# Kernel tuning notes

Hardware: AMD Instinct MI355X
Metric: run time of the kernel (lower is better)

Reference implementation:

```python
import jax, jax.numpy as jnp
import numpy as np

S = 2   # scale_factor
K = 5   # k_up
M = 48  # m_channels
KE = 3  # k_encoder


def conv2d(x, w, b, pad):
    # NCHW conv, stride 1, symmetric padding (matches nn.Conv2d(padding=pad))
    y = jax.lax.conv_general_dilated(
        x, w, window_strides=(1, 1), padding=[(pad, pad), (pad, pad)],
        dimension_numbers=("NCHW", "OIHW", "NCHW"))
    return y + b[None, :, None, None]


def setup_inputs() -> dict:
    key = jax.random.key(0)
    k1, k2, k3, k4, k5 = jax.random.split(key, 5)
    C_in = 64
    x = jax.random.normal(k1, (8, C_in, 128, 128), dtype=jnp.float32)
    w_compress = jax.random.normal(k2, (M, C_in, 1, 1), dtype=jnp.float32) * 0.1
    b_compress = jax.random.normal(k3, (M,), dtype=jnp.float32) * 0.05
    w_encoder = jax.random.normal(k4, ((K * S) ** 2, M, KE, KE), dtype=jnp.float32) * 0.05
    b_encoder = jax.random.normal(k5, ((K * S) ** 2,), dtype=jnp.float32) * 0.05
    return {"x": x, "w_compress": w_compress, "b_compress": b_compress,
            "w_encoder": w_encoder, "b_encoder": b_encoder}


def reference(x, w_compress, b_compress, w_encoder, b_encoder):
    B, C, H, W = x.shape
    # mask branch: compress -> relu -> encoder -> softmax over k_up^2
    y = jax.nn.relu(conv2d(x, w_compress, b_compress, pad=0))
    y = conv2d(y, w_encoder, b_encoder, pad=KE // 2)          # [B, (K*S)^2, H, W]
    y = y.reshape(B, S * S, K * K, H, W)
    y = jax.nn.softmax(y, axis=2)
    # unfold x with kernel K, pad K//2, stride 1 -> [B, C, K*K, H, W]
    p = K // 2
    xpad = jnp.pad(x, ((0, 0), (0, 0), (p, p), (p, p)))
    unf = jnp.stack([xpad[:, :, i:i + H, j:j + W]
                     for i in range(K) for j in range(K)], axis=2)
    # per-subpixel softmax-weighted patch sum; channel layout (scale_idx, C)
    out = jnp.einsum("bskhw,bckhw->bschw", y, unf)            # [B, S^2, C, H, W]
    out = out.reshape(B, S * S * C, H, W)
    # PixelShuffle(S): view (B, C_out, r, r, H, W) -> (B, C_out, H, r, W, r)
    r = S
    c_out = (S * S * C) // (r * r)
    out = out.reshape(B, c_out, r, r, H, W).transpose(0, 1, 4, 2, 5, 3)
    return out.reshape(B, c_out, H * r, W * r)
```

## Files before the change

### kernel.cpp

```cpp
#include <hip/hip_runtime.h>

#define HW 16384

typedef __bf16 bf16x8 __attribute__((ext_vector_type(8)));
typedef __bf16 bf16x4 __attribute__((ext_vector_type(4)));
typedef float  f32x4  __attribute__((ext_vector_type(4)));
typedef float  f32x2  __attribute__((ext_vector_type(2)));

__global__ __launch_bounds__(256)
void prep_xt(const float* __restrict__ x, __bf16* __restrict__ xt) {
    __shared__ float lds[256 * 65];
    const int b = blockIdx.x & 7, chunk = blockIdx.x >> 3;
    const int t = threadIdx.x;
    const int pos0 = chunk * 256;
    const float* xb = x + (size_t)b * 64 * HW + pos0;
    for (int c = 0; c < 64; ++c)
        lds[t * 65 + c] = xb[(size_t)c * HW + t];
    __syncthreads();
    const int q = t & 3, pp = t >> 2;
    #pragma unroll
    for (int it = 0; it < 4; ++it) {
        int pos = it * 64 + pp;
        __bf16* o = xt + ((size_t)b * HW + pos0 + pos) * 64 + q * 16;
        bf16x8 v0, v1;
        #pragma unroll
        for (int e = 0; e < 8; ++e) {
            v0[e] = (__bf16)lds[pos * 65 + q * 16 + e];
            v1[e] = (__bf16)lds[pos * 65 + q * 16 + 8 + e];
        }
        *(bf16x8*)o       = v0;
        *(bf16x8*)(o + 8) = v1;
    }
}

__global__ __launch_bounds__(256)
void prep_w(const float* __restrict__ we, const float* __restrict__ wc,
            __bf16* __restrict__ wt, __bf16* __restrict__ wcb) {
    int idx = blockIdx.x * 256 + threadIdx.x;
    if (idx < 112 * 448) {
        int e = idx / 448, k = idx % 448;
        float v = 0.f;
        if (e < 100 && k < 432) {
            int t = k / 48, m = k % 48;
            v = we[(e * 48 + m) * 9 + t];
        }
        wt[idx] = (__bf16)v;
    } else {
        idx -= 112 * 448;
        if (idx < 48 * 64) wcb[idx] = (__bf16)wc[idx];
    }
}

__global__ __launch_bounds__(256, 2)
void carafe_weights(const __bf16* __restrict__ xt,
                    const __bf16* __restrict__ wcb, const float* __restrict__ bc,
                    const __bf16* __restrict__ wt, const float* __restrict__ be,
                    unsigned int* __restrict__ wnp) {
    __shared__ __align__(16) char smem[59392];
    __bf16*    y1  = (__bf16*)smem;
    _Float16*  lgt = (_Float16*)smem;

    const int tid = threadIdx.x;
    const int lane = tid & 63, wv = tid >> 6;
    const int lgp = lane >> 4, lr = lane & 15;
    const int b = blockIdx.x & 7, tile = blockIdx.x >> 3;
    const int h0 = (tile >> 3) << 4, w0 = (tile & 7) << 4;

    {
        bf16x8 bw[3][2];
        float bias1[3];
        #pragma unroll
        for (int nt = 0; nt < 3; ++nt) {
            bias1[nt] = bc[nt * 16 + lr];
            #pragma unroll
            for (int kc = 0; kc < 2; ++kc)
                bw[nt][kc] = *(const bf16x8*)(wcb + (nt * 16 + lr) * 64 + kc * 32 + lgp * 8);
        }
        for (int pt = wv; pt < 21; pt += 4) {
            int pos = pt * 16 + lr;
            int pr = (pos * 1821) >> 15;  int pc = pos - pr * 18;
            int hy = h0 - 1 + pr, wx = w0 - 1 + pc;
            bool ok = (hy >= 0) & (hy < 128) & (wx >= 0) & (wx < 128);
            const __bf16* ap = xt + ((size_t)b * HW + (ok ? (hy * 128 + wx) : 0)) * 64 + lgp * 8;
            bf16x8 a0 = *(const bf16x8*)ap;
            bf16x8 a1 = *(const bf16x8*)(ap + 32);
            if (!ok) {
                #pragma unroll
                for (int e = 0; e < 8; ++e) { a0[e] = (__bf16)0.f; a1[e] = (__bf16)0.f; }
            }
            #pragma unroll
            for (int nt = 0; nt < 3; ++nt) {
                f32x4 cc = {bias1[nt], bias1[nt], bias1[nt], bias1[nt]};
                cc = __builtin_amdgcn_mfma_f32_16x16x32_bf16(a0, bw[nt][0], cc, 0, 0, 0);
                cc = __builtin_amdgcn_mfma_f32_16x16x32_bf16(a1, bw[nt][1], cc, 0, 0, 0);
                #pragma unroll
                for (int r = 0; r < 4; ++r) {
                    int posw = pt * 16 + lgp * 4 + r;
                    int pr2 = (posw * 1821) >> 15;  int pc2 = posw - pr2 * 18;
                    int hy2 = h0 - 1 + pr2, wx2 = w0 - 1 + pc2;
                    bool ok2 = (hy2 >= 0) & (hy2 < 128) & (wx2 >= 0) & (wx2 < 128);
                    float v = ok2 ? fmaxf(cc[r], 0.f) : 0.f;
                    y1[posw * 56 + nt * 16 + lr] = (__bf16)v;
                }
            }
        }
    }
    for (int i = tid; i < 448; i += 256)
        y1[336 * 56 + i] = (__bf16)0.f;
    __syncthreads();

    f32x4 acc[4][7];
    #pragma unroll
    for (int ot = 0; ot < 7; ++ot) {
        int o_ = ot * 16 + lr;
        float bz = (o_ < 100) ? be[o_] : 0.f;
        #pragma unroll
        for (int i = 0; i < 4; ++i) acc[i][ot] = {bz, bz, bz, bz};
    }
    const int ptg0 = wv * 4;

    auto ldA = [&](bf16x8 A[4], int kc) {
        int Kb = kc * 32 + lgp * 8;
        int t  = (Kb * 683) >> 15;  int m0 = Kb - t * 48;
        int ty = (t * 11) >> 5;     int tx = t - ty * 3;
        int base = ty * 18 + lr + tx;
        #pragma unroll
        for (int i = 0; i < 4; ++i)
            A[i] = *(const bf16x8*)(y1 + ((ptg0 + i) * 18 + base) * 56 + m0);
    };
    auto ldB = [&](bf16x8 B[7], int kc) {
        #pragma unroll
        for (int j = 0; j < 7; ++j)
            B[j] = *(const bf16x8*)(wt + (j * 16 + lr) * 448 + kc * 32 + lgp * 8);
    };
    auto mm = [&](bf16x8 A[4], bf16x8 B[7]) {
        #pragma unroll
        for (int i = 0; i < 4; ++i)
            #pragma unroll
            for (int j = 0; j < 7; ++j)
                acc[i][j] = __builtin_amdgcn_mfma_f32_16x16x32_bf16(A[i], B[j], acc[i][j], 0, 0, 0);
    };

    bf16x8 A0[4], B0[7], A1[4], B1[7];
    ldA(A0, 0); ldB(B0, 0);
    #pragma unroll
    for (int kc = 0; kc < 14; kc += 2) {
        if (kc + 1 < 14) { ldA(A1, kc + 1); ldB(B1, kc + 1); }
        mm(A0, B0);
        if (kc + 2 < 14) { ldA(A0, kc + 2); ldB(B0, kc + 2); }
        if (kc + 1 < 14) mm(A1, B1);
    }
    __syncthreads();

    #pragma unroll
    for (int i = 0; i < 4; ++i)
        #pragma unroll
        for (int j = 0; j < 7; ++j) {
            int o_ = j * 16 + lr;
            #pragma unroll
            for (int r = 0; r < 4; ++r) {
                int p = (ptg0 + i) * 16 + lgp * 4 + r;
                lgt[p * 116 + o_] = (_Float16)acc[i][j][r];
            }
        }
    __syncthreads();

    const int p = tid;
    const _Float16* lrow = lgt + p * 116;
    #pragma unroll
    for (int s2 = 0; s2 < 2; ++s2) {
        unsigned int* wp = wnp + (size_t)(b * 2 + s2) * 25 * HW + tile * 256 + p;
        #pragma unroll
        for (int k = 0; k < 25; ++k) {
            unsigned short lo = __builtin_bit_cast(unsigned short, lrow[(2 * s2) * 25 + k]);
            unsigned short hi = __builtin_bit_cast(unsigned short, lrow[(2 * s2 + 1) * 25 + k]);
            wp[(size_t)k * HW] = (unsigned int)lo | ((unsigned int)hi << 16);
        }
    }
}

__global__ __launch_bounds__(512, 4)
void carafe_apply(const __bf16* __restrict__ xt, const unsigned int* __restrict__ wnp,
                  float* __restrict__ out) {
    __shared__ __bf16 lx[400 * 68];

    const int tid = threadIdx.x;
    const int b = blockIdx.x & 7, tile = blockIdx.x >> 3;
    const int h0 = (tile >> 3) << 4, w0 = (tile & 7) << 4;

    const int l8 = tid & 7, pg = tid >> 3;
    bf16x8 hv[7];
    #pragma unroll
    for (int it = 0; it < 7; ++it) {
        int pos = it * 64 + pg;
        bf16x8 v = {};
        if (pos < 400) {
            int r = pos / 20, q = pos % 20;
            int hy = h0 - 2 + r, wx = w0 - 2 + q;
            if (hy >= 0 && hy < 128 && wx >= 0 && wx < 128)
                v = *(const bf16x8*)(xt + ((size_t)b * HW + hy * 128 + wx) * 64 + l8 * 8);
        }
        hv[it] = v;
    }

    const int pix = tid & 255, sgrp = tid >> 8;
    const int py = pix >> 4, px = pix & 15;
    const int h = h0 + py, w = w0 + px;
    float wt_[50];
    {
        const unsigned int* wp = wnp + (size_t)(b * 2 + sgrp) * 25 * HW + tile * 256 + pix;
        #pragma unroll
        for (int k = 0; k < 25; ++k) {
            unsigned int u = wp[(size_t)k * HW];
            wt_[k]      = (float)__builtin_bit_cast(_Float16, (unsigned short)(u & 0xffffu));
            wt_[25 + k] = (float)__builtin_bit_cast(_Float16, (unsigned short)(u >> 16));
        }
        #pragma unroll
        for (int g = 0; g < 2; ++g) {
            float* v = wt_ + g * 25;
            float mx = v[0];
            #pragma unroll
            for (int k = 1; k < 25; ++k) mx = fmaxf(mx, v[k]);
            float s = 0.f;
            #pragma unroll
            for (int k = 0; k < 25; ++k) { v[k] = __expf(v[k] - mx); s += v[k]; }
            float inv = 1.f / s;
            #pragma unroll
            for (int k = 0; k < 25; ++k) v[k] *= inv;
        }
    }

    #pragma unroll
    for (int it = 0; it < 7; ++it) {
        int pos = it * 64 + pg;
        if (pos < 400) {
            bf16x4 vlo = {hv[it][0], hv[it][1], hv[it][2], hv[it][3]};
            bf16x4 vhi = {hv[it][4], hv[it][5], hv[it][6], hv[it][7]};
            *(bf16x4*)(lx + pos * 68 + l8 * 8)     = vlo;
            *(bf16x4*)(lx + pos * 68 + l8 * 8 + 4) = vhi;
        }
    }
    __syncthreads();

    float* ob = out + (size_t)b * 256 * HW;
    #pragma unroll 1
    for (int cq = 0; cq < 16; ++cq) {
        f32x2 a0 = {0.f, 0.f}, a1 = {0.f, 0.f}, a2 = {0.f, 0.f}, a3 = {0.f, 0.f};
        #pragma unroll
        for (int ki = 0; ki < 5; ++ki) {
            const int rowbase = (py + ki) * 20 + px;
            #pragma unroll
            for (int kj = 0; kj < 5; ++kj) {
                uint2 u = *(const uint2*)(lx + (rowbase + kj) * 68 + cq * 4);
                f32x2 xlo = { __uint_as_float(u.x << 16), __uint_as_float(u.x & 0xffff0000u) };
                f32x2 xhi = { __uint_as_float(u.y << 16), __uint_as_float(u.y & 0xffff0000u) };
                float wA = wt_[ki * 5 + kj];
                float wB = wt_[25 + ki * 5 + kj];
                a0 += xlo * wA;
                a1 += xhi * wA;
                a2 += xlo * wB;
                a3 += xhi * wB;
            }
        }
        size_t base0 = ((size_t)(sgrp * 32 + cq) * 256 + 2 * h) * 256 + 2 * w;
        *(f32x2*)(ob + base0)       = a0;
        *(f32x2*)(ob + base0 + 256) = a1;
        size_t base1 = base0 + (size_t)16 * 256 * 256;
        *(f32x2*)(ob + base1)       = a2;
        *(f32x2*)(ob + base1 + 256) = a3;
    }
}

extern "C" void kernel_launch(void* const* d_in, const int* in_sizes, int n_in,
                              void* d_out, int out_size, void* d_ws, size_t ws_size,
                              hipStream_t stream) {
    const float* x  = (const float*)d_in[0];
    const float* wc = (const float*)d_in[1];
    const float* bc = (const float*)d_in[2];
    const float* we = (const float*)d_in[3];
    const float* be = (const float*)d_in[4];
    float* out = (float*)d_out;

    __bf16*       xt  = (__bf16*)d_ws;
    __bf16*       wte = (__bf16*)((char*)d_ws + 16777216);
    __bf16*       wcb = (__bf16*)((char*)d_ws + 16777216 + 100352);
    unsigned int* wnp = (unsigned int*)((char*)d_ws + 16883712);

    prep_xt<<<512, 256, 0, stream>>>(x, xt);
    prep_w<<<208, 256, 0, stream>>>(we, wc, wte, wcb);
    carafe_weights<<<512, 256, 0, stream>>>(xt, wcb, bc, wte, be, wnp);
    carafe_apply<<<512, 512, 0, stream>>>(xt, wnp, out);
}
```

Baseline: 92.64 us.

## Split encoder output channels across two blocks per tile to raise occupancy

The weights kernel now launches twice as many blocks, each computing half of the 100 encoder outputs (two subpixel groups) for a tile, cutting accumulators from 4x7 to 4x4 MFMA tiles and shrinking LDS so four blocks fit per CU. The compress stage is transposed so each lane writes four contiguous channels with a vector store and reuses the load-time bounds check. The output stores in the apply kernel become nontemporal. The cost is that each half recomputes the compress conv and reloads the input halo, and the software double-buffering of the K loop is replaced by a plain unroll-by-two loop.

```diff
diff --git a/kernel.cpp b/kernel.cpp
--- a/kernel.cpp
+++ b/kernel.cpp
@@ -37,7 +37,7 @@
 void prep_w(const float* __restrict__ we, const float* __restrict__ wc,
             __bf16* __restrict__ wt, __bf16* __restrict__ wcb) {
     int idx = blockIdx.x * 256 + threadIdx.x;
-    if (idx < 112 * 448) {
+    if (idx < 128 * 448) {
         int e = idx / 448, k = idx % 448;
         float v = 0.f;
         if (e < 100 && k < 432) {
@@ -46,32 +46,34 @@
         }
         wt[idx] = (__bf16)v;
     } else {
-        idx -= 112 * 448;
+        idx -= 128 * 448;
         if (idx < 48 * 64) wcb[idx] = (__bf16)wc[idx];
     }
 }
 
-__global__ __launch_bounds__(256, 2)
+__global__ __launch_bounds__(256, 4)
 void carafe_weights(const __bf16* __restrict__ xt,
                     const __bf16* __restrict__ wcb, const float* __restrict__ bc,
                     const __bf16* __restrict__ wt, const float* __restrict__ be,
                     unsigned int* __restrict__ wnp) {
-    __shared__ __align__(16) char smem[59392];
+    __shared__ __align__(16) char smem[38528];
     __bf16*    y1  = (__bf16*)smem;
     _Float16*  lgt = (_Float16*)smem;
 
     const int tid = threadIdx.x;
     const int lane = tid & 63, wv = tid >> 6;
     const int lgp = lane >> 4, lr = lane & 15;
-    const int b = blockIdx.x & 7, tile = blockIdx.x >> 3;
+    const int b = blockIdx.x & 7;
+    const int rst = blockIdx.x >> 3;
+    const int tile = rst >> 1, half = rst & 1;
     const int h0 = (tile >> 3) << 4, w0 = (tile & 7) << 4;
 
     {
         bf16x8 bw[3][2];
-        float bias1[3];
+        f32x4 bias4[3];
         #pragma unroll
         for (int nt = 0; nt < 3; ++nt) {
-            bias1[nt] = bc[nt * 16 + lr];
+            bias4[nt] = *(const f32x4*)(bc + nt * 16 + lgp * 4);
             #pragma unroll
             for (int kc = 0; kc < 2; ++kc)
                 bw[nt][kc] = *(const bf16x8*)(wcb + (nt * 16 + lr) * 64 + kc * 32 + lgp * 8);
@@ -90,18 +92,16 @@
             }
             #pragma unroll
             for (int nt = 0; nt < 3; ++nt) {
-                f32x4 cc = {bias1[nt], bias1[nt], bias1[nt], bias1[nt]};
-                cc = __builtin_amdgcn_mfma_f32_16x16x32_bf16(a0, bw[nt][0], cc, 0, 0, 0);
-                cc = __builtin_amdgcn_mfma_f32_16x16x32_bf16(a1, bw[nt][1], cc, 0, 0, 0);
+                f32x4 cc = {0.f, 0.f, 0.f, 0.f};
+                cc = __builtin_amdgcn_mfma_f32_16x16x32_bf16(bw[nt][0], a0, cc, 0, 0, 0);
+                cc = __builtin_amdgcn_mfma_f32_16x16x32_bf16(bw[nt][1], a1, cc, 0, 0, 0);
+                bf16x4 o4;
                 #pragma unroll
                 for (int r = 0; r < 4; ++r) {
-                    int posw = pt * 16 + lgp * 4 + r;
-                    int pr2 = (posw * 1821) >> 15;  int pc2 = posw - pr2 * 18;
-                    int hy2 = h0 - 1 + pr2, wx2 = w0 - 1 + pc2;
-                    bool ok2 = (hy2 >= 0) & (hy2 < 128) & (wx2 >= 0) & (wx2 < 128);
-                    float v = ok2 ? fmaxf(cc[r], 0.f) : 0.f;
-                    y1[posw * 56 + nt * 16 + lr] = (__bf16)v;
+                    float v = ok ? fmaxf(cc[r] + bias4[nt][r], 0.f) : 0.f;
+                    o4[r] = (__bf16)v;
                 }
+                *(bf16x4*)(y1 + pos * 56 + nt * 16 + lgp * 4) = o4;
             }
         }
     }
@@ -109,73 +109,58 @@
         y1[336 * 56 + i] = (__bf16)0.f;
     __syncthreads();
 
-    f32x4 acc[4][7];
-    #pragma unroll
-    for (int ot = 0; ot < 7; ++ot) {
-        int o_ = ot * 16 + lr;
+    const int ob0 = half * 50;
+    f32x4 acc[4][4];
+    #pragma unroll
+    for (int j = 0; j < 4; ++j) {
+        int o_ = ob0 + j * 16 + lr;
         float bz = (o_ < 100) ? be[o_] : 0.f;
         #pragma unroll
-        for (int i = 0; i < 4; ++i) acc[i][ot] = {bz, bz, bz, bz};
+        for (int i = 0; i < 4; ++i) acc[i][j] = {bz, bz, bz, bz};
     }
     const int ptg0 = wv * 4;
 
-    auto ldA = [&](bf16x8 A[4], int kc) {
+    #pragma unroll 2
+    for (int kc = 0; kc < 14; ++kc) {
         int Kb = kc * 32 + lgp * 8;
         int t  = (Kb * 683) >> 15;  int m0 = Kb - t * 48;
         int ty = (t * 11) >> 5;     int tx = t - ty * 3;
         int base = ty * 18 + lr + tx;
+        bf16x8 A[4], B[4];
         #pragma unroll
         for (int i = 0; i < 4; ++i)
             A[i] = *(const bf16x8*)(y1 + ((ptg0 + i) * 18 + base) * 56 + m0);
-    };
-    auto ldB = [&](bf16x8 B[7], int kc) {
-        #pragma unroll
-        for (int j = 0; j < 7; ++j)
-            B[j] = *(const bf16x8*)(wt + (j * 16 + lr) * 448 + kc * 32 + lgp * 8);
-    };
-    auto mm = [&](bf16x8 A[4], bf16x8 B[7]) {
+        #pragma unroll
+        for (int j = 0; j < 4; ++j)
+            B[j] = *(const bf16x8*)(wt + (ob0 + j * 16 + lr) * 448 + kc * 32 + lgp * 8);
         #pragma unroll
         for (int i = 0; i < 4; ++i)
             #pragma unroll
-            for (int j = 0; j < 7; ++j)
+            for (int j = 0; j < 4; ++j)
                 acc[i][j] = __builtin_amdgcn_mfma_f32_16x16x32_bf16(A[i], B[j], acc[i][j], 0, 0, 0);
-    };
-
-    bf16x8 A0[4], B0[7], A1[4], B1[7];
-    ldA(A0, 0); ldB(B0, 0);
-    #pragma unroll
-    for (int kc = 0; kc < 14; kc += 2) {
-        if (kc + 1 < 14) { ldA(A1, kc + 1); ldB(B1, kc + 1); }
-        mm(A0, B0);
-        if (kc + 2 < 14) { ldA(A0, kc + 2); ldB(B0, kc + 2); }
-        if (kc + 1 < 14) mm(A1, B1);
     }
     __syncthreads();
 
     #pragma unroll
     for (int i = 0; i < 4; ++i)
         #pragma unroll
-        for (int j = 0; j < 7; ++j) {
+        for (int j = 0; j < 4; ++j) {
             int o_ = j * 16 + lr;
             #pragma unroll
             for (int r = 0; r < 4; ++r) {
                 int p = (ptg0 + i) * 16 + lgp * 4 + r;
-                lgt[p * 116 + o_] = (_Float16)acc[i][j][r];
-            }
-        }
-    __syncthreads();
-
-    const int p = tid;
-    const _Float16* lrow = lgt + p * 116;
-    #pragma unroll
-    for (int s2 = 0; s2 < 2; ++s2) {
-        unsigned int* wp = wnp + (size_t)(b * 2 + s2) * 25 * HW + tile * 256 + p;
-        #pragma unroll
-        for (int k = 0; k < 25; ++k) {
-            unsigned short lo = __builtin_bit_cast(unsigned short, lrow[(2 * s2) * 25 + k]);
-            unsigned short hi = __builtin_bit_cast(unsigned short, lrow[(2 * s2 + 1) * 25 + k]);
-            wp[(size_t)k * HW] = (unsigned int)lo | ((unsigned int)hi << 16);
-        }
+                lgt[p * 66 + o_] = (_Float16)acc[i][j][r];
+            }
+        }
+    __syncthreads();
+
+    const _Float16* lrow = lgt + tid * 66;
+    unsigned int* wp = wnp + (size_t)(b * 2 + half) * 25 * HW + tile * 256 + tid;
+    #pragma unroll
+    for (int k = 0; k < 25; ++k) {
+        unsigned short lo = __builtin_bit_cast(unsigned short, lrow[k]);
+        unsigned short hi = __builtin_bit_cast(unsigned short, lrow[25 + k]);
+        wp[(size_t)k * HW] = (unsigned int)lo | ((unsigned int)hi << 16);
     }
 }
 
@@ -263,11 +248,11 @@
             }
         }
         size_t base0 = ((size_t)(sgrp * 32 + cq) * 256 + 2 * h) * 256 + 2 * w;
-        *(f32x2*)(ob + base0)       = a0;
-        *(f32x2*)(ob + base0 + 256) = a1;
         size_t base1 = base0 + (size_t)16 * 256 * 256;
-        *(f32x2*)(ob + base1)       = a2;
-        *(f32x2*)(ob + base1 + 256) = a3;
+        __builtin_nontemporal_store(a0, (f32x2*)(ob + base0));
+        __builtin_nontemporal_store(a1, (f32x2*)(ob + base0 + 256));
+        __builtin_nontemporal_store(a2, (f32x2*)(ob + base1));
+        __builtin_nontemporal_store(a3, (f32x2*)(ob + base1 + 256));
     }
 }
 
@@ -283,11 +268,11 @@
 
     __bf16*       xt  = (__bf16*)d_ws;
     __bf16*       wte = (__bf16*)((char*)d_ws + 16777216);
-    __bf16*       wcb = (__bf16*)((char*)d_ws + 16777216 + 100352);
-    unsigned int* wnp = (unsigned int*)((char*)d_ws + 16883712);
+    __bf16*       wcb = (__bf16*)((char*)d_ws + 16777216 + 114688);
+    unsigned int* wnp = (unsigned int*)((char*)d_ws + 16777216 + 114688 + 6144);
 
     prep_xt<<<512, 256, 0, stream>>>(x, xt);
-    prep_w<<<208, 256, 0, stream>>>(we, wc, wte, wcb);
-    carafe_weights<<<512, 256, 0, stream>>>(xt, wcb, bc, wte, be, wnp);
+    prep_w<<<236, 256, 0, stream>>>(we, wc, wte, wcb);
+    carafe_weights<<<1024, 256, 0, stream>>>(xt, wcb, bc, wte, be, wnp);
     carafe_apply<<<512, 512, 0, stream>>>(xt, wnp, out);
 }
```

After: 92.62 us. Within noise of the previous version (-0.0%).

## Fuse 1x1 compress conv into transpose prep, store y1 to global

Applied to the files above, without the earlier changes.

The 1x1 compress conv with ReLU moves out of carafe_weights and into the x-transpose prep kernel. Each compressed activation is now computed once per pixel and written to a global bf16 buffer, where before it was recomputed for the halo pixels of every 16x16 tile. carafe_weights then just loads the y1 halo tile with zero padding. The change also unrolls the apply loop by two and uses nontemporal stores for the output, at the cost of an extra 25MB global buffer write and read.

```diff
diff --git a/kernel.cpp b/kernel.cpp
--- a/kernel.cpp
+++ b/kernel.cpp
@@ -8,36 +8,10 @@
 typedef float  f32x2  __attribute__((ext_vector_type(2)));
 
 __global__ __launch_bounds__(256)
-void prep_xt(const float* __restrict__ x, __bf16* __restrict__ xt) {
-    __shared__ float lds[256 * 65];
-    const int b = blockIdx.x & 7, chunk = blockIdx.x >> 3;
-    const int t = threadIdx.x;
-    const int pos0 = chunk * 256;
-    const float* xb = x + (size_t)b * 64 * HW + pos0;
-    for (int c = 0; c < 64; ++c)
-        lds[t * 65 + c] = xb[(size_t)c * HW + t];
-    __syncthreads();
-    const int q = t & 3, pp = t >> 2;
-    #pragma unroll
-    for (int it = 0; it < 4; ++it) {
-        int pos = it * 64 + pp;
-        __bf16* o = xt + ((size_t)b * HW + pos0 + pos) * 64 + q * 16;
-        bf16x8 v0, v1;
-        #pragma unroll
-        for (int e = 0; e < 8; ++e) {
-            v0[e] = (__bf16)lds[pos * 65 + q * 16 + e];
-            v1[e] = (__bf16)lds[pos * 65 + q * 16 + 8 + e];
-        }
-        *(bf16x8*)o       = v0;
-        *(bf16x8*)(o + 8) = v1;
-    }
-}
-
-__global__ __launch_bounds__(256)
 void prep_w(const float* __restrict__ we, const float* __restrict__ wc,
             __bf16* __restrict__ wt, __bf16* __restrict__ wcb) {
     int idx = blockIdx.x * 256 + threadIdx.x;
-    if (idx < 112 * 448) {
+    if (idx < 128 * 448) {
         int e = idx / 448, k = idx % 448;
         float v = 0.f;
         if (e < 100 && k < 432) {
@@ -46,14 +20,97 @@
         }
         wt[idx] = (__bf16)v;
     } else {
-        idx -= 112 * 448;
+        idx -= 128 * 448;
         if (idx < 48 * 64) wcb[idx] = (__bf16)wc[idx];
     }
 }
 
 __global__ __launch_bounds__(256, 2)
-void carafe_weights(const __bf16* __restrict__ xt,
-                    const __bf16* __restrict__ wcb, const float* __restrict__ bc,
+void prep_xty1(const float* __restrict__ x, const __bf16* __restrict__ wcb,
+               const float* __restrict__ bc,
+               __bf16* __restrict__ xt, __bf16* __restrict__ y1o) {
+    __shared__ __align__(16) float lds[256 * 65];
+    __bf16* y1s = (__bf16*)lds;
+
+    const int b = blockIdx.x & 7, chunk = blockIdx.x >> 3;
+    const int t = threadIdx.x;
+    const int lane = t & 63, wv = t >> 6;
+    const int lgp = lane >> 4, lr = lane & 15;
+    const int pos0 = chunk * 256;
+
+    const float* xb = x + (size_t)b * 64 * HW + pos0;
+    for (int c = 0; c < 64; ++c)
+        lds[t * 65 + c] = xb[(size_t)c * HW + t];
+    __syncthreads();
+
+    {
+        const int q = t & 3, pp = t >> 2;
+        #pragma unroll
+        for (int it = 0; it < 4; ++it) {
+            int pos = it * 64 + pp;
+            __bf16* o = xt + ((size_t)b * HW + pos0 + pos) * 64 + q * 16;
+            bf16x8 v0, v1;
+            #pragma unroll
+            for (int e = 0; e < 8; ++e) {
+                v0[e] = (__bf16)lds[pos * 65 + q * 16 + e];
+                v1[e] = (__bf16)lds[pos * 65 + q * 16 + 8 + e];
+            }
+            *(bf16x8*)o       = v0;
+            *(bf16x8*)(o + 8) = v1;
+        }
+    }
+    bf16x8 af[4][2];
+    #pragma unroll
+    for (int i = 0; i < 4; ++i) {
+        int pix = (wv * 4 + i) * 16 + lr;
+        #pragma unroll
+        for (int kc = 0; kc < 2; ++kc)
+            #pragma unroll
+            for (int e = 0; e < 8; ++e)
+                af[i][kc][e] = (__bf16)lds[pix * 65 + kc * 32 + lgp * 8 + e];
+    }
+    __syncthreads();
+
+    {
+        bf16x8 bw[3][2];
+        f32x4 bias4[3];
+        #pragma unroll
+        for (int nt = 0; nt < 3; ++nt) {
+            bias4[nt] = *(const f32x4*)(bc + nt * 16 + lgp * 4);
+            #pragma unroll
+            for (int kc = 0; kc < 2; ++kc)
+                bw[nt][kc] = *(const bf16x8*)(wcb + (nt * 16 + lr) * 64 + kc * 32 + lgp * 8);
+        }
+        #pragma unroll
+        for (int i = 0; i < 4; ++i) {
+            int pix = (wv * 4 + i) * 16 + lr;
+            #pragma unroll
+            for (int nt = 0; nt < 3; ++nt) {
+                f32x4 cc = bias4[nt];
+                cc = __builtin_amdgcn_mfma_f32_16x16x32_bf16(bw[nt][0], af[i][0], cc, 0, 0, 0);
+                cc = __builtin_amdgcn_mfma_f32_16x16x32_bf16(bw[nt][1], af[i][1], cc, 0, 0, 0);
+                bf16x4 o4;
+                #pragma unroll
+                for (int r = 0; r < 4; ++r) o4[r] = (__bf16)fmaxf(cc[r], 0.f);
+                *(bf16x4*)(y1s + pix * 56 + nt * 16 + lgp * 4) = o4;
+            }
+        }
+    }
+    __syncthreads();
+
+    __bf16* yo = y1o + (size_t)(b * HW + pos0) * 48;
+    #pragma unroll
+    for (int i = 0; i < 6; ++i) {
+        int c = i * 256 + t;
+        int pix = (c * 10923) >> 16;
+        int mc  = c - pix * 6;
+        bf16x8 v = *(bf16x8*)(y1s + pix * 56 + mc * 8);
+        *(bf16x8*)(yo + (size_t)c * 8) = v;
+    }
+}
+
+__global__ __launch_bounds__(256, 2)
+void carafe_weights(const __bf16* __restrict__ y1g,
                     const __bf16* __restrict__ wt, const float* __restrict__ be,
                     unsigned int* __restrict__ wnp) {
     __shared__ __align__(16) char smem[59392];
@@ -66,47 +123,24 @@
     const int b = blockIdx.x & 7, tile = blockIdx.x >> 3;
     const int h0 = (tile >> 3) << 4, w0 = (tile & 7) << 4;
 
-    {
-        bf16x8 bw[3][2];
-        float bias1[3];
-        #pragma unroll
-        for (int nt = 0; nt < 3; ++nt) {
-            bias1[nt] = bc[nt * 16 + lr];
-            #pragma unroll
-            for (int kc = 0; kc < 2; ++kc)
-                bw[nt][kc] = *(const bf16x8*)(wcb + (nt * 16 + lr) * 64 + kc * 32 + lgp * 8);
-        }
-        for (int pt = wv; pt < 21; pt += 4) {
-            int pos = pt * 16 + lr;
-            int pr = (pos * 1821) >> 15;  int pc = pos - pr * 18;
-            int hy = h0 - 1 + pr, wx = w0 - 1 + pc;
-            bool ok = (hy >= 0) & (hy < 128) & (wx >= 0) & (wx < 128);
-            const __bf16* ap = xt + ((size_t)b * HW + (ok ? (hy * 128 + wx) : 0)) * 64 + lgp * 8;
-            bf16x8 a0 = *(const bf16x8*)ap;
-            bf16x8 a1 = *(const bf16x8*)(ap + 32);
-            if (!ok) {
-                #pragma unroll
-                for (int e = 0; e < 8; ++e) { a0[e] = (__bf16)0.f; a1[e] = (__bf16)0.f; }
-            }
-            #pragma unroll
-            for (int nt = 0; nt < 3; ++nt) {
-                f32x4 cc = {bias1[nt], bias1[nt], bias1[nt], bias1[nt]};
-                cc = __builtin_amdgcn_mfma_f32_16x16x32_bf16(a0, bw[nt][0], cc, 0, 0, 0);
-                cc = __builtin_amdgcn_mfma_f32_16x16x32_bf16(a1, bw[nt][1], cc, 0, 0, 0);
-                #pragma unroll
-                for (int r = 0; r < 4; ++r) {
-                    int posw = pt * 16 + lgp * 4 + r;
-                    int pr2 = (posw * 1821) >> 15;  int pc2 = posw - pr2 * 18;
-                    int hy2 = h0 - 1 + pr2, wx2 = w0 - 1 + pc2;
-                    bool ok2 = (hy2 >= 0) & (hy2 < 128) & (wx2 >= 0) & (wx2 < 128);
-                    float v = ok2 ? fmaxf(cc[r], 0.f) : 0.f;
-                    y1[posw * 56 + nt * 16 + lr] = (__bf16)v;
-                }
-            }
-        }
-    }
-    for (int i = tid; i < 448; i += 256)
-        y1[336 * 56 + i] = (__bf16)0.f;
+    const __bf16* y1b = y1g + (size_t)b * HW * 48;
+    #pragma unroll
+    for (int it = 0; it < 8; ++it) {
+        int id = it * 256 + tid;
+        if (id < 1944) {
+            int hr  = (id * 607) >> 16;
+            int rem = id - hr * 108;
+            int wc  = (rem * 10923) >> 16;
+            int mc  = rem - wc * 6;
+            int hy = h0 - 1 + hr, wx = w0 - 1 + wc;
+            bf16x8 v = {};
+            if (hy >= 0 && hy < 128 && wx >= 0 && wx < 128)
+                v = *(const bf16x8*)(y1b + (size_t)(hy * 128 + wx) * 48 + mc * 8);
+            *(bf16x8*)(y1 + (hr * 18 + wc) * 56 + mc * 8) = v;
+        }
+    }
+    for (int i = tid; i < 1120; i += 256)
+        y1[324 * 56 + i] = (__bf16)0.f;
     __syncthreads();
 
     f32x4 acc[4][7];
@@ -165,11 +199,10 @@
         }
     __syncthreads();
 
-    const int p = tid;
-    const _Float16* lrow = lgt + p * 116;
+    const _Float16* lrow = lgt + tid * 116;
     #pragma unroll
     for (int s2 = 0; s2 < 2; ++s2) {
-        unsigned int* wp = wnp + (size_t)(b * 2 + s2) * 25 * HW + tile * 256 + p;
+        unsigned int* wp = wnp + (size_t)(b * 2 + s2) * 25 * HW + tile * 256 + tid;
         #pragma unroll
         for (int k = 0; k < 25; ++k) {
             unsigned short lo = __builtin_bit_cast(unsigned short, lrow[(2 * s2) * 25 + k]);
@@ -243,7 +276,7 @@
     __syncthreads();
 
     float* ob = out + (size_t)b * 256 * HW;
-    #pragma unroll 1
+    #pragma unroll 2
     for (int cq = 0; cq < 16; ++cq) {
         f32x2 a0 = {0.f, 0.f}, a1 = {0.f, 0.f}, a2 = {0.f, 0.f}, a3 = {0.f, 0.f};
         #pragma unroll
@@ -263,11 +296,11 @@
             }
         }
         size_t base0 = ((size_t)(sgrp * 32 + cq) * 256 + 2 * h) * 256 + 2 * w;
-        *(f32x2*)(ob + base0)       = a0;
-        *(f32x2*)(ob + base0 + 256) = a1;
         size_t base1 = base0 + (size_t)16 * 256 * 256;
-        *(f32x2*)(ob + base1)       = a2;
-        *(f32x2*)(ob + base1 + 256) = a3;
+        __builtin_nontemporal_store(a0, (f32x2*)(ob + base0));
+        __builtin_nontemporal_store(a1, (f32x2*)(ob + base0 + 256));
+        __builtin_nontemporal_store(a2, (f32x2*)(ob + base1));
+        __builtin_nontemporal_store(a3, (f32x2*)(ob + base1 + 256));
     }
 }
 
@@ -282,12 +315,13 @@
     float* out = (float*)d_out;
 
     __bf16*       xt  = (__bf16*)d_ws;
-    __bf16*       wte = (__bf16*)((char*)d_ws + 16777216);
-    __bf16*       wcb = (__bf16*)((char*)d_ws + 16777216 + 100352);
-    unsigned int* wnp = (unsigned int*)((char*)d_ws + 16883712);
-
-    prep_xt<<<512, 256, 0, stream>>>(x, xt);
-    prep_w<<<208, 256, 0, stream>>>(we, wc, wte, wcb);
-    carafe_weights<<<512, 256, 0, stream>>>(xt, wcb, bc, wte, be, wnp);
+    __bf16*       y1g = (__bf16*)((char*)d_ws + 16777216);
+    __bf16*       wte = (__bf16*)((char*)d_ws + 41943040);
+    __bf16*       wcb = (__bf16*)((char*)d_ws + 41943040 + 114688);
+    unsigned int* wnp = (unsigned int*)((char*)d_ws + 41943040 + 114688 + 6144);
+
+    prep_w<<<236, 256, 0, stream>>>(we, wc, wte, wcb);
+    prep_xty1<<<512, 256, 0, stream>>>(x, wcb, bc, xt, y1g);
+    carafe_weights<<<512, 256, 0, stream>>>(y1g, wte, be, wnp);
     carafe_apply<<<512, 512, 0, stream>>>(xt, wnp, out);
 }
```

After: 195.2 us, median of 2. 111% more time.
